# Kernel tuning notes

Hardware: AMD Instinct MI355X
Metric: run time of the kernel (lower is better)

Reference implementation:

```python
import jax, jax.numpy as jnp
import numpy as np

G, IN_DIM, OUT_DIM = 100000, 256, 128
B, N = 4096, 8192
ALPHA = 0.2          # LeakyReLU negative slope
NEG_INF = -9e15      # same masking constant as the torch module
EPS = 1e-12          # F.normalize eps


def setup_inputs() -> dict:
    key = jax.random.key(0)
    k1, k2, k3, k4, k5, k6, k7 = jax.random.split(key, 7)
    global_feature = jax.random.normal(k1, (G, IN_DIM), dtype=jnp.float32)
    nodes = jax.random.randint(k2, (B,), 0, G, dtype=jnp.int32)
    unique_nodes = jax.random.randint(k3, (N,), 0, G, dtype=jnp.int32)
    mask = jax.random.randint(k4, (B, N), 0, 2, dtype=jnp.int32)
    # ensure every row has at least one neighbor (original always includes self)
    mask = mask.at[:, 0].set(1)
    # xavier_uniform with gain=1.414
    gain = 1.414
    lim_W = gain * np.sqrt(6.0 / (IN_DIM + OUT_DIM))
    W = jax.random.uniform(k5, (IN_DIM, OUT_DIM), jnp.float32, -lim_W, lim_W)
    lim_a = gain * np.sqrt(6.0 / (2 * OUT_DIM + 1))
    a1 = jax.random.uniform(k6, (OUT_DIM,), jnp.float32, -lim_a, lim_a)
    a2 = jax.random.uniform(k7, (OUT_DIM,), jnp.float32, -lim_a, lim_a)
    return {"global_feature": global_feature, "nodes": nodes,
            "unique_nodes": unique_nodes, "mask": mask,
            "W": W, "a1": a1, "a2": a2}


def reference(global_feature, nodes, unique_nodes, mask, W, a1, a2):
    # project gathered features: [B,F], [N,F]
    h_nodes = global_feature[nodes] @ W
    h_neigh = global_feature[unique_nodes] @ W
    # additive attention scores; equivalent to cat([h_i,h_j]) @ a
    e = h_nodes @ a1[:, None] + (h_neigh @ a2)[None, :]   # [B,N]
    e = jnp.where(e >= 0, e, ALPHA * e)                    # leaky relu
    e = jnp.where(mask > 0, e, NEG_INF)
    attention = jax.nn.softmax(e, axis=1)                  # [B,N]
    out = attention @ h_neigh                              # [B,F]
    norm = jnp.linalg.norm(out, axis=1, keepdims=True)
    out = out / jnp.maximum(norm, EPS)                     # F.normalize p=2
    return out
```

## Files before the change

kernel.cpp:

```cpp
#include <hip/hip_runtime.h>
#include <hip/hip_bf16.h>

#define IN_DIM  256
#define OUT_DIM 128
#define B_ROWS  4096
#define N_COLS  8192
#define ALPHA   0.2f
#define NS      16

typedef unsigned short u16;
typedef unsigned int   u32;
typedef __attribute__((ext_vector_type(8))) short short8;
typedef __attribute__((ext_vector_type(4))) float floatx4;

__device__ __forceinline__ float bf2f(u16 v){ return __uint_as_float(((u32)v) << 16); }
__device__ __forceinline__ float bflo(u32 v){ return __uint_as_float(v << 16); }
__device__ __forceinline__ float bfhi(u32 v){ return __uint_as_float(v & 0xffff0000u); }
__device__ __forceinline__ u16 f2bf(float f){
    u32 u = __float_as_uint(f);
    u += 0x7fffu + ((u >> 16) & 1u);
    return (u16)(u >> 16);
}
__device__ __forceinline__ u32 pack_bf16(float a, float b){
    __hip_bfloat162 h = __float22bfloat162_rn(make_float2(a, b));
    return *reinterpret_cast<u32*>(&h);
}

__device__ __forceinline__ int detect_bf16_wave(const u32* __restrict__ g){
    int lane = threadIdx.x & 63;
    uint4 u = ((const uint4*)g)[lane];
#define CHK(x) ((((x) >> 7) & 0xFF) >= 110 && (((x) >> 7) & 0xFF) <= 140)
    unsigned long long c0 = __ballot(CHK(u.x)), c1 = __ballot(CHK(u.y));
    unsigned long long c2 = __ballot(CHK(u.z)), c3 = __ballot(CHK(u.w));
#undef CHK
    int votes = __popcll(c0) + __popcll(c1) + __popcll(c2) + __popcll(c3);
    return votes >= 128;
}

__global__ __launch_bounds__(128) void k_prep(const void* __restrict__ gf,
                                              const void* __restrict__ W, const void* __restrict__ a1,
                                              const void* __restrict__ a2,
                                              u16* __restrict__ WB, float* __restrict__ Wa1,
                                              float* __restrict__ a2f){
    const int isbf = detect_bf16_wave((const u32*)gf);
    const int c  = threadIdx.x;
    const int kb = blockIdx.x;
    float a1c = isbf ? bf2f(((const u16*)a1)[c]) : ((const float*)a1)[c];
    float w[8]; short8 v;
#pragma unroll
    for (int j = 0; j < 8; j++){
        w[j] = isbf ? bf2f(((const u16*)W)[(kb*8 + j) * OUT_DIM + c])
                    : ((const float*)W)[(kb*8 + j) * OUT_DIM + c];
        v[j] = (short)f2bf(w[j]);
    }
    ((short8*)WB)[kb * OUT_DIM + c] = v;

    __shared__ float red[2][8];
    int lane = c & 63, wv = c >> 6;
#pragma unroll
    for (int j = 0; j < 8; j++){
        float p = w[j] * a1c;
        p += __shfl_xor(p, 1);  p += __shfl_xor(p, 2);  p += __shfl_xor(p, 4);
        p += __shfl_xor(p, 8);  p += __shfl_xor(p, 16); p += __shfl_xor(p, 32);
        if (lane == 0) red[wv][j] = p;
    }
    __syncthreads();
    if (c < 8) Wa1[kb*8 + c] = red[0][c] + red[1][c];
    if (kb == 0) a2f[c] = isbf ? bf2f(((const u16*)a2)[c]) : ((const float*)a2)[c];
}

#define HN_BLKS 512
#define ESN_BLKS 1024
#define ZERO_BLKS 128
__global__ __launch_bounds__(256) void k_mid(const void* __restrict__ gf, const int* __restrict__ uniq,
                                             const int* __restrict__ nodes,
                                             const u16* __restrict__ WB, const float* __restrict__ a2f,
                                             const float* __restrict__ Wa1,
                                             u16* __restrict__ hB, float2* __restrict__ esg2,
                                             float2* __restrict__ esn2, float* __restrict__ oacc){
    const int bid = blockIdx.x;
    const int t   = threadIdx.x;

    if (bid < HN_BLKS){
        const int n0   = bid * 16;
        const int lane = t & 63;
        const int wv   = t >> 6;
        const int q    = lane >> 4;
        const int m    = lane & 15;
        const int isbf = detect_bf16_wave((const u32*)gf);
        const int jb0  = wv * 2;

        const size_t row = (size_t)uniq[n0 + m];
        const short8* wb8 = (const short8*)WB;

        floatx4 acc0 = {0.f,0.f,0.f,0.f};
        floatx4 acc1 = {0.f,0.f,0.f,0.f};

#pragma unroll
        for (int ks = 0; ks < IN_DIM/32; ks++){
            short8 afrag;
            if (isbf){
                afrag = *(const short8*)((const u16*)gf + row * IN_DIM + ks*32 + q*8);
            } else {
                const float* gp = (const float*)gf + row * IN_DIM + ks*32 + q*8;
                float4 f0 = *(const float4*)gp;
                float4 f1 = *(const float4*)(gp + 4);
                afrag[0] = (short)f2bf(f0.x); afrag[1] = (short)f2bf(f0.y);
                afrag[2] = (short)f2bf(f0.z); afrag[3] = (short)f2bf(f0.w);
                afrag[4] = (short)f2bf(f1.x); afrag[5] = (short)f2bf(f1.y);
                afrag[6] = (short)f2bf(f1.z); afrag[7] = (short)f2bf(f1.w);
            }
            const int kb = ks*4 + q;
            short8 b0 = wb8[kb * OUT_DIM + jb0*16 + m];
            short8 b1 = wb8[kb * OUT_DIM + (jb0+1)*16 + m];
            acc0 = __builtin_amdgcn_mfma_f32_16x16x32_bf16(afrag, b0, acc0, 0, 0, 0);
            acc1 = __builtin_amdgcn_mfma_f32_16x16x32_bf16(afrag, b1, acc1, 0, 0, 0);
        }

        {
            uint2 v0, v1;
            v0.x = pack_bf16(acc0[0], acc0[1]);
            v0.y = pack_bf16(acc0[2], acc0[3]);
            v1.x = pack_bf16(acc1[0], acc1[1]);
            v1.y = pack_bf16(acc1[2], acc1[3]);
            u16* base = hB + (size_t)(n0/8 + (q>>1)) * 1024 + (q&1)*4;
            *(uint2*)(base + (jb0*16 + m) * 8)     = v0;
            *(uint2*)(base + ((jb0+1)*16 + m) * 8) = v1;
        }

        __shared__ float sred[4][16];
        float a2c0 = a2f[jb0*16 + m], a2c1 = a2f[(jb0+1)*16 + m];
#pragma unroll
        for (int reg = 0; reg < 4; reg++){
            float pr = acc0[reg]*a2c0 + acc1[reg]*a2c1;
            pr += __shfl_xor(pr, 1); pr += __shfl_xor(pr, 2);
            pr += __shfl_xor(pr, 4); pr += __shfl_xor(pr, 8);
            if (m == 0) sred[wv][q*4 + reg] = pr;
        }
        __syncthreads();
        if (t < 16){
            float s = sred[0][t] + sred[1][t] + sred[2][t] + sred[3][t];
            s = fminf(fmaxf(s, -40.f), 40.f);
            esg2[n0 + t] = make_float2(__expf(s), __expf(ALPHA * s));
        }
    } else if (bid < HN_BLKS + ESN_BLKS){
        const int eb = bid - HN_BLKS;
        int lane = t & 63, wv = t >> 6;
        int b = eb * 4 + wv;
        const int isbf = detect_bf16_wave((const u32*)gf);
        float4 wa = ((const float4*)Wa1)[lane];
        float x0, x1, x2, x3;
        if (isbf){
            uint2 gg = ((const uint2*)((const u16*)gf + (size_t)nodes[b] * IN_DIM))[lane];
            x0 = bflo(gg.x); x1 = bfhi(gg.x); x2 = bflo(gg.y); x3 = bfhi(gg.y);
        } else {
            float4 gg = ((const float4*)((const float*)gf + (size_t)nodes[b] * IN_DIM))[lane];
            x0 = gg.x; x1 = gg.y; x2 = gg.z; x3 = gg.w;
        }
        float s = x0*wa.x + x1*wa.y + x2*wa.z + x3*wa.w;
        s += __shfl_xor(s, 1);  s += __shfl_xor(s, 2);  s += __shfl_xor(s, 4);
        s += __shfl_xor(s, 8);  s += __shfl_xor(s, 16); s += __shfl_xor(s, 32);
        if (lane == 0){
            s = fminf(fmaxf(s, -40.f), 40.f);
            esn2[b] = make_float2(__expf(s), __expf(ALPHA * s));
        }
    } else {
        const int zb = bid - (HN_BLKS + ESN_BLKS);
        float4* dst = (float4*)(oacc + (size_t)zb * (B_ROWS*OUT_DIM/ZERO_BLKS));
        float4 z = {0.f,0.f,0.f,0.f};
#pragma unroll
        for (int i = 0; i < 4; i++)
            dst[t + i*256] = z;
    }
}

__global__ __launch_bounds__(128, 4) void k_attn(const int* __restrict__ mask,
                                                 const float2* __restrict__ esn2,
                                                 const float2* __restrict__ esg2,
                                                 const u16* __restrict__ hB,
                                                 float* __restrict__ oacc){
    const int bid = blockIdx.x;
    const int ns  = bid & (NS-1);
    const int rg  = bid >> 4;
    const int t = threadIdx.x, lane = t & 63, wv = t >> 6;
    const int q = lane >> 4, m = lane & 15;
    const int rowbase = rg*32 + wv*16;
    const int row = rowbase + m;
    const int n0  = ns * (N_COLS/NS);

    __shared__ float4 seg[256];
    {
        const float4* egsrc = (const float4*)esg2 + (n0 >> 1);
        seg[t]       = egsrc[t];
        seg[t + 128] = egsrc[t + 128];
    }
    __syncthreads();

    const float2 en = esn2[row];
    const float enx = en.x, eny = en.y;
    const int* mrow = mask + (size_t)row * N_COLS;
    const short8* hb8 = (const short8*)hB;

    floatx4 acc[8];
#pragma unroll
    for (int jb = 0; jb < 8; jb++){ floatx4 z = {0.f,0.f,0.f,0.f}; acc[jb] = z; }

#pragma unroll 4
    for (int ks = 0; ks < 16; ks++){
        const int nn = n0 + ks*32;
        int4 ma = *(const int4*)(mrow + nn + q*8);
        int4 mb = *(const int4*)(mrow + nn + q*8 + 4);
        const float4* egl = &seg[ks*16 + q*4];
        float4 g0 = egl[0], g1 = egl[1], g2 = egl[2], g3 = egl[3];

        float p[8];
#define PEL(j, mk, gx, gy) { float tt = fmaxf(enx * (gx), eny * (gy)); \
                             p[j] = (mk) ? tt : 0.f; }
        PEL(0, ma.x, g0.x, g0.y) PEL(1, ma.y, g0.z, g0.w)
        PEL(2, ma.z, g1.x, g1.y) PEL(3, ma.w, g1.z, g1.w)
        PEL(4, mb.x, g2.x, g2.y) PEL(5, mb.y, g2.z, g2.w)
        PEL(6, mb.z, g3.x, g3.y) PEL(7, mb.w, g3.z, g3.w)
#undef PEL
        uint4 av;
        av.x = pack_bf16(p[0], p[1]); av.y = pack_bf16(p[2], p[3]);
        av.z = pack_bf16(p[4], p[5]); av.w = pack_bf16(p[6], p[7]);
        short8 af = *reinterpret_cast<short8*>(&av);

        const int kb = (nn >> 3) + q;
#pragma unroll
        for (int jb = 0; jb < 8; jb++){
            short8 bfr = hb8[kb * OUT_DIM + jb*16 + m];
            acc[jb] = __builtin_amdgcn_mfma_f32_16x16x32_bf16(af, bfr, acc[jb], 0, 0, 0);
        }
    }

#pragma unroll
    for (int jb = 0; jb < 8; jb++)
#pragma unroll
        for (int reg = 0; reg < 4; reg++)
            atomicAdd(&oacc[(size_t)(rowbase + q*4 + reg) * OUT_DIM + jb*16 + m], acc[jb][reg]);
}

__global__ __launch_bounds__(128) void k_norm(const float* __restrict__ oacc,
                                              const void* __restrict__ gf, void* __restrict__ out){
    const int isbf = detect_bf16_wave((const u32*)gf);
    const int b = blockIdx.x, c = threadIdx.x;
    float v = oacc[(size_t)b * OUT_DIM + c];
    float ss = v * v;
    for (int off = 32; off > 0; off >>= 1) ss += __shfl_down(ss, off);
    __shared__ float red[2];
    int lane = c & 63, wv = c >> 6;
    if (lane == 0) red[wv] = ss;
    __syncthreads();
    float tot = red[0] + red[1];
    float scale = 1.f / fmaxf(sqrtf(tot), 1e-12f);
    float o = v * scale;
    if (isbf) ((u16*)out)[(size_t)b * OUT_DIM + c] = f2bf(o);
    else      ((float*)out)[(size_t)b * OUT_DIM + c] = o;
}

extern "C" void kernel_launch(void* const* d_in, const int* in_sizes, int n_in,
                              void* d_out, int out_size, void* d_ws, size_t ws_size,
                              hipStream_t stream){
    const void* gf    = d_in[0];
    const int*  nodes = (const int*)d_in[1];
    const int*  uniq  = (const int*)d_in[2];
    const int*  mask  = (const int*)d_in[3];
    const void* W     = d_in[4];
    const void* a1    = d_in[5];
    const void* a2    = d_in[6];

    char* ws = (char*)d_ws;
    u16*    hB   = (u16*)ws;
    u16*    WB   = (u16*)(ws + (2u<<20));
    float2* esg2 = (float2*)(ws + (2u<<20) + (64u<<10));
    float*  Wa1  = (float*)(ws + (2u<<20) + (128u<<10));
    float*  a2f  = (float*)(ws + (2u<<20) + (129u<<10));
    float2* esn2 = (float2*)(ws + (2u<<20) + (130u<<10));
    float*  oacc = (float*)(ws + (4u<<20));

    hipLaunchKernelGGL(k_prep, dim3(32), dim3(128), 0, stream, gf, W, a1, a2, WB, Wa1, a2f);
    hipLaunchKernelGGL(k_mid,  dim3(HN_BLKS + ESN_BLKS + ZERO_BLKS), dim3(256), 0, stream,
                       gf, uniq, nodes, WB, a2f, Wa1, hB, esg2, esn2, oacc);
    hipLaunchKernelGGL(k_attn, dim3((B_ROWS/32)*NS), dim3(128), 0, stream, mask, esn2, esg2, hB, oacc);
    hipLaunchKernelGGL(k_norm, dim3(B_ROWS), dim3(128), 0, stream, oacc, gf, d_out);
}
```

Baseline: 297.2 us.

## Pre-pack int32 attention mask into a bitmap before the attention kernel

Adds a packing phase to the mid kernel that turns the 128 MB int32 mask into a 4 MB bitmap, one bit per entry. The attention kernel then reads one 32-bit word per 32 columns instead of two int4 loads per lane. The total mask bytes read stay the same, but they move into a streaming pass that runs alongside the projection blocks, which leaves the MFMA loop with much lighter memory traffic. It only activates when the workspace holds at least 10 MB, and the packing loads use a per-lane stride that may coalesce poorly.

```diff
diff --git a/kernel.cpp b/kernel.cpp
--- a/kernel.cpp
+++ b/kernel.cpp
@@ -10,6 +10,7 @@
 
 typedef unsigned short u16;
 typedef unsigned int   u32;
+typedef unsigned long long u64;
 typedef __attribute__((ext_vector_type(8))) short short8;
 typedef __attribute__((ext_vector_type(4))) float floatx4;
 
@@ -69,6 +70,7 @@
     if (kb == 0) a2f[c] = isbf ? bf2f(((const u16*)a2)[c]) : ((const float*)a2)[c];
 }
 
+#define PK_BLKS 512
 #define HN_BLKS 512
 #define ESN_BLKS 1024
 #define ZERO_BLKS 128
@@ -77,9 +79,30 @@
                                              const u16* __restrict__ WB, const float* __restrict__ a2f,
                                              const float* __restrict__ Wa1,
                                              u16* __restrict__ hB, float2* __restrict__ esg2,
-                                             float2* __restrict__ esn2, float* __restrict__ oacc){
-    const int bid = blockIdx.x;
-    const int t   = threadIdx.x;
+                                             float2* __restrict__ esn2, float* __restrict__ oacc,
+                                             const int* __restrict__ mask, u64* __restrict__ pb,
+                                             int pk_blks){
+    const int bid0 = blockIdx.x;
+    const int t    = threadIdx.x;
+
+    if (bid0 < pk_blks){
+        const size_t u0 = ((size_t)bid0 * 256 + t) * 4;
+        const uint4* src = (const uint4*)mask;
+#pragma unroll
+        for (int r = 0; r < 4; r++){
+            const size_t u = u0 + r;
+            u64 accb = 0;
+#pragma unroll
+            for (int i = 0; i < 16; i++){
+                uint4 v = src[u*16 + i];
+                u32 nib = (v.x ? 1u : 0u) | (v.y ? 2u : 0u) | (v.z ? 4u : 0u) | (v.w ? 8u : 0u);
+                accb |= (u64)nib << (i*4);
+            }
+            pb[u] = accb;
+        }
+        return;
+    }
+    const int bid = bid0 - pk_blks;
 
     if (bid < HN_BLKS){
         const int n0   = bid * 16;
@@ -174,7 +197,9 @@
     }
 }
 
+template<int USE_PB>
 __global__ __launch_bounds__(128, 4) void k_attn(const int* __restrict__ mask,
+                                                 const u32* __restrict__ pb32,
                                                  const float2* __restrict__ esn2,
                                                  const float2* __restrict__ esg2,
                                                  const u16* __restrict__ hB,
@@ -199,6 +224,7 @@
     const float2 en = esn2[row];
     const float enx = en.x, eny = en.y;
     const int* mrow = mask + (size_t)row * N_COLS;
+    const u32* pmrow = pb32 + ((size_t)row * (N_COLS/32) + ns * 16);
     const short8* hb8 = (const short8*)hB;
 
     floatx4 acc[8];
@@ -208,19 +234,31 @@
 #pragma unroll 4
     for (int ks = 0; ks < 16; ks++){
         const int nn = n0 + ks*32;
-        int4 ma = *(const int4*)(mrow + nn + q*8);
-        int4 mb = *(const int4*)(mrow + nn + q*8 + 4);
         const float4* egl = &seg[ks*16 + q*4];
         float4 g0 = egl[0], g1 = egl[1], g2 = egl[2], g3 = egl[3];
 
         float p[8];
+        if (USE_PB){
+            const u32 w = pmrow[ks];
+            const u32 mbyte = (w >> (q*8)) & 0xffu;
+#define PELB(j, gx, gy) { float tt = fmaxf(enx * (gx), eny * (gy)); \
+                          p[j] = (mbyte & (1u << (j))) ? tt : 0.f; }
+            PELB(0, g0.x, g0.y) PELB(1, g0.z, g0.w)
+            PELB(2, g1.x, g1.y) PELB(3, g1.z, g1.w)
+            PELB(4, g2.x, g2.y) PELB(5, g2.z, g2.w)
+            PELB(6, g3.x, g3.y) PELB(7, g3.z, g3.w)
+#undef PELB
+        } else {
+            int4 ma = *(const int4*)(mrow + nn + q*8);
+            int4 mb = *(const int4*)(mrow + nn + q*8 + 4);
 #define PEL(j, mk, gx, gy) { float tt = fmaxf(enx * (gx), eny * (gy)); \
                              p[j] = (mk) ? tt : 0.f; }
-        PEL(0, ma.x, g0.x, g0.y) PEL(1, ma.y, g0.z, g0.w)
-        PEL(2, ma.z, g1.x, g1.y) PEL(3, ma.w, g1.z, g1.w)
-        PEL(4, mb.x, g2.x, g2.y) PEL(5, mb.y, g2.z, g2.w)
-        PEL(6, mb.z, g3.x, g3.y) PEL(7, mb.w, g3.z, g3.w)
+            PEL(0, ma.x, g0.x, g0.y) PEL(1, ma.y, g0.z, g0.w)
+            PEL(2, ma.z, g1.x, g1.y) PEL(3, ma.w, g1.z, g1.w)
+            PEL(4, mb.x, g2.x, g2.y) PEL(5, mb.y, g2.z, g2.w)
+            PEL(6, mb.z, g3.x, g3.y) PEL(7, mb.w, g3.z, g3.w)
 #undef PEL
+        }
         uint4 av;
         av.x = pack_bf16(p[0], p[1]); av.y = pack_bf16(p[2], p[3]);
         av.z = pack_bf16(p[4], p[5]); av.w = pack_bf16(p[6], p[7]);
@@ -278,10 +316,19 @@
     float*  a2f  = (float*)(ws + (2u<<20) + (129u<<10));
     float2* esn2 = (float2*)(ws + (2u<<20) + (130u<<10));
     float*  oacc = (float*)(ws + (4u<<20));
+    u64*    pb   = (u64*)(ws + (6u<<20));
+
+    const int use_pb = (ws_size >= (10u << 20)) ? 1 : 0;
+    const int pk = use_pb ? PK_BLKS : 0;
 
     hipLaunchKernelGGL(k_prep, dim3(32), dim3(128), 0, stream, gf, W, a1, a2, WB, Wa1, a2f);
-    hipLaunchKernelGGL(k_mid,  dim3(HN_BLKS + ESN_BLKS + ZERO_BLKS), dim3(256), 0, stream,
-                       gf, uniq, nodes, WB, a2f, Wa1, hB, esg2, esn2, oacc);
-    hipLaunchKernelGGL(k_attn, dim3((B_ROWS/32)*NS), dim3(128), 0, stream, mask, esn2, esg2, hB, oacc);
+    hipLaunchKernelGGL(k_mid,  dim3(pk + HN_BLKS + ESN_BLKS + ZERO_BLKS), dim3(256), 0, stream,
+                       gf, uniq, nodes, WB, a2f, Wa1, hB, esg2, esn2, oacc, mask, pb, pk);
+    if (use_pb)
+        hipLaunchKernelGGL(k_attn<1>, dim3((B_ROWS/32)*NS), dim3(128), 0, stream,
+                           mask, (const u32*)pb, esn2, esg2, hB, oacc);
+    else
+        hipLaunchKernelGGL(k_attn<0>, dim3((B_ROWS/32)*NS), dim3(128), 0, stream,
+                           mask, (const u32*)pb, esn2, esg2, hB, oacc);
     hipLaunchKernelGGL(k_norm, dim3(B_ROWS), dim3(128), 0, stream, oacc, gf, d_out);
 }
```

New measurement: 311.1 us. +4.7%, slower.
